# Performance work log

Measured on AMD Instinct MI355X. Metric: run time of the kernel, lower is better.

Reference implementation:

```python
import jax, jax.numpy as jnp
import numpy as np

B, T, D, H = 32, 1024, 128, 4
DH = D // H  # per-head dim = 32
NEG = -(2.0**32) + 1.0  # padding value used by SoftmaxWeightedSum
LN_EPS = 1e-9


def setup_inputs() -> dict:
    key = jax.random.key(0)
    k1, k2, k3, k4 = jax.random.split(key, 4)
    x = jax.random.normal(k1, (B, T, D), dtype=jnp.float32)
    keys_length = jax.random.randint(k2, (B, 1), 1, T + 1, dtype=jnp.int32)
    W = jax.random.normal(k3, (D, 3 * D), dtype=jnp.float32) * 0.05
    W_output = jax.random.normal(k4, (D, D), dtype=jnp.float32) * 0.05
    gamma = jnp.ones((D,), dtype=jnp.float32)
    beta = jnp.zeros((D,), dtype=jnp.float32)
    return {"x": x, "keys_length": keys_length, "W": W,
            "W_output": W_output, "gamma": gamma, "beta": beta}


def reference(x, keys_length, W, W_output, gamma, beta):
    # QKV projection: [B,T,D] @ [D,3D] -> [B,T,3D]
    qkv = jnp.einsum('btd,de->bte', x, W)
    q, k, v = jnp.split(qkv, 3, axis=-1)

    # tf.split(axis=2)+concat(axis=0) == head-major [H,B,T,DH]
    def to_heads(t):
        return t.reshape(B, T, H, DH).transpose(2, 0, 1, 3)
    q, k, v = to_heads(q), to_heads(k), to_heads(v)

    # DotAttention with scale by sqrt(per-head key dim)
    scores = jnp.einsum('hbqd,hbkd->hbqk', q, k) / jnp.sqrt(jnp.float32(DH))

    # key padding mask from sequence lengths: [B,T] bool
    key_mask = jnp.arange(T)[None, :] < keys_length  # keys_length is [B,1]
    # causal (future_binding) lower-triangular mask: [T,T]
    causal = jnp.tril(jnp.ones((T, T), dtype=bool))
    mask = causal[None, None, :, :] & key_mask[None, :, None, :]  # [1,B,T,T] -> broadcast over H
    scores = jnp.where(mask, scores, NEG)

    attn = jax.nn.softmax(scores, axis=-1)  # [H,B,T,T]
    out = jnp.einsum('hbqk,hbkd->hbqd', attn, v)  # [H,B,T,DH]

    # concat heads back to channel dim: [B,T,D]
    out = out.transpose(1, 2, 0, 3).reshape(B, T, D)
    out = jnp.einsum('btd,de->bte', out, W_output)

    # residual + layernorm (dropout is identity at inference)
    out = out + x
    mean = jnp.mean(out, axis=-1, keepdims=True)
    var = jnp.var(out, axis=-1, keepdims=True)
    out = (out - mean) * jax.lax.rsqrt(var + LN_EPS) * gamma + beta
    return out
```

## Files before the change

kernel.cpp:

```cpp
#include <hip/hip_runtime.h>
#include <hip/hip_bf16.h>

#define B_ 32
#define T_ 1024
#define D_ 128
#define H_ 4
#define DH_ 32

typedef unsigned short ushort_t;
typedef unsigned int uint_t;
typedef unsigned short ushort4_t __attribute__((ext_vector_type(4)));
typedef unsigned short ushort8_t __attribute__((ext_vector_type(8)));
typedef short short8_t __attribute__((ext_vector_type(8)));
typedef float float4_t __attribute__((ext_vector_type(4)));

__device__ __forceinline__ ushort_t f2bf_bits(float f) {
    __hip_bfloat16 h = __float2bfloat16(f);
    return *reinterpret_cast<ushort_t*>(&h);
}
__device__ __forceinline__ uint_t pk_bf16(float hi, float lo) {
    return __builtin_amdgcn_perm(__float_as_uint(hi), __float_as_uint(lo),
                                 0x07060302u);
}
#if __has_builtin(__builtin_amdgcn_exp2f)
__device__ __forceinline__ float fast_exp2(float x) { return __builtin_amdgcn_exp2f(x); }
#else
__device__ __forceinline__ float fast_exp2(float x) { return exp2f(x); }
#endif

__global__ __launch_bounds__(256) void transpose_weights(
    const float* __restrict__ W, const float* __restrict__ Wo,
    ushort_t* __restrict__ Wt, ushort_t* __restrict__ Wot)
{
    const int id = blockIdx.x * 256 + threadIdx.x;
    if (id < 128 * 384) {
        const int n = id >> 7, k = id & 127;
        Wt[id] = f2bf_bits(W[(size_t)k * 384 + n]);
    } else {
        const int id2 = id - 128 * 384;
        const int n = id2 >> 7, k = id2 & 127;
        Wot[id2] = f2bf_bits(Wo[(size_t)k * 128 + n]);
    }
}

__global__ __launch_bounds__(256) void qkv_mfma(
    const float* __restrict__ x, const ushort_t* __restrict__ Wt,
    __hip_bfloat16* __restrict__ qws, __hip_bfloat16* __restrict__ kws,
    __hip_bfloat16* __restrict__ vtws)
{
    __shared__ ushort_t qkA[2][16 * 200];
    __shared__ ushort_t qkB[2][16 * 72];

    const int tid = threadIdx.x;
    const int lane = tid & 63;
    const int i15 = lane & 15, quad = lane >> 4;
    const int wid = tid >> 6;
    const int wpart = wid & 1;
    const int pairIdx = wid >> 1;
    const int gw = blockIdx.x * 4 + wid;
    const int row0 = (gw >> 1) * 32;

    short8_t af[2][4];
    #pragma unroll
    for (int rg = 0; rg < 2; ++rg) {
        #pragma unroll
        for (int kc = 0; kc < 4; ++kc) {
            const float4 x0 = *(const float4*)(x + (size_t)(row0 + rg * 16 + i15) * 128 + kc * 32 + quad * 8);
            const float4 x1 = *(const float4*)(x + (size_t)(row0 + rg * 16 + i15) * 128 + kc * 32 + quad * 8 + 4);
            short8_t a;
            a[0] = (short)f2bf_bits(x0.x); a[1] = (short)f2bf_bits(x0.y);
            a[2] = (short)f2bf_bits(x0.z); a[3] = (short)f2bf_bits(x0.w);
            a[4] = (short)f2bf_bits(x1.x); a[5] = (short)f2bf_bits(x1.y);
            a[6] = (short)f2bf_bits(x1.z); a[7] = (short)f2bf_bits(x1.w);
            af[rg][kc] = a;
        }
    }

    float4_t acc[2][12];
    #pragma unroll
    for (int rg = 0; rg < 2; ++rg)
        #pragma unroll
        for (int nt = 0; nt < 12; ++nt) acc[rg][nt] = (float4_t){0.f, 0.f, 0.f, 0.f};

    #pragma unroll
    for (int nt = 0; nt < 12; ++nt) {
        const int n = wpart * 192 + nt * 16 + i15;
        const ushort_t* wb = Wt + (size_t)n * 128 + quad * 8;
        #pragma unroll
        for (int kc = 0; kc < 4; ++kc) {
            const short8_t bf = *(const short8_t*)(wb + kc * 32);
            acc[0][nt] = __builtin_amdgcn_mfma_f32_16x16x32_bf16(af[0][kc], bf, acc[0][nt], 0, 0, 0);
            acc[1][nt] = __builtin_amdgcn_mfma_f32_16x16x32_bf16(af[1][kc], bf, acc[1][nt], 0, 0, 0);
        }
    }

    const float scale = 0.17677669529663687f * 1.4426950408889634f;
    const int t = lane >> 2, c4 = lane & 3;

    #pragma unroll
    for (int rg = 0; rg < 2; ++rg) {
        const int r0 = row0 + rg * 16;
        const int b = r0 >> 10, t0 = r0 & 1023;
        if (wpart == 0) {
            ushort_t* Ls = qkA[pairIdx];
            #pragma unroll
            for (int nt = 0; nt < 12; ++nt) {
                const int col = nt * 16 + i15;
                const float sc = (nt < 8) ? scale : 1.f;
                #pragma unroll
                for (int r = 0; r < 4; ++r)
                    Ls[(quad * 4 + r) * 200 + col] = f2bf_bits(acc[rg][nt][r] * sc);
            }
            #pragma unroll
            for (int it = 0; it < 6; ++it) {
                const int col8 = it * 4 + c4;
                const ushort8_t v8 = *(const ushort8_t*)(Ls + t * 200 + col8 * 8);
                __hip_bfloat16* base = (it < 4) ? qws : kws;
                const int h = (it < 4) ? it : (it - 4);
                *(ushort8_t*)((ushort_t*)base +
                    ((size_t)(b * H_ + h) * T_ + t0 + t) * DH_ + c4 * 8) = v8;
            }
        } else {
            ushort_t* Ls = qkB[pairIdx];
            #pragma unroll
            for (int nt = 0; nt < 12; ++nt) {
                if (nt < 4) {
                    const int col = nt * 16 + i15;
                    #pragma unroll
                    for (int r = 0; r < 4; ++r)
                        Ls[(quad * 4 + r) * 72 + col] = f2bf_bits(acc[rg][nt][r]);
                } else {
                    const int ch = nt * 16 + i15 - 64;
                    const int h = ch >> 5, dh = ch & 31;
                    ushort4_t pk;
                    #pragma unroll
                    for (int r = 0; r < 4; ++r) pk[r] = f2bf_bits(acc[rg][nt][r]);
                    *(ushort4_t*)((ushort_t*)vtws +
                        ((size_t)(b * H_ + h) * DH_ + dh) * T_ + t0 + quad * 4) = pk;
                }
            }
            #pragma unroll
            for (int it = 0; it < 2; ++it) {
                const int col8 = it * 4 + c4;
                const ushort8_t v8 = *(const ushort8_t*)(Ls + t * 72 + col8 * 8);
                *(ushort8_t*)((ushort_t*)kws +
                    ((size_t)(b * H_ + 2 + it) * T_ + t0 + t) * DH_ + c4 * 8) = v8;
            }
        }
    }
}

__global__ __launch_bounds__(256) void attn_proj_ln(
    const ushort_t* __restrict__ qws, const ushort_t* __restrict__ kws,
    const ushort_t* __restrict__ vtws, const int* __restrict__ keys_length,
    const ushort_t* __restrict__ Wot, const float* __restrict__ x,
    const float* __restrict__ gamma, const float* __restrict__ beta,
    float* __restrict__ out)
{
    __shared__ ushort_t plds[4][32 * 72];
    __shared__ ushort_t att[32 * 128];

    const int wid = threadIdx.x >> 6;
    const int lane = threadIdx.x & 63;
    const int i15 = lane & 15, quad = lane >> 4;
    const int b = blockIdx.x & 31;
    const int st = 31 - (blockIdx.x >> 5);
    const int qbase = st * 32;
    const int h = wid;
    const int bh = b * 4 + h;
    const int len = keys_length[b];

    const ushort_t* Qb = qws + (size_t)bh * T_ * DH_;
    const ushort_t* Kb = kws + (size_t)bh * T_ * DH_;
    const ushort_t* Vtb = vtws + (size_t)bh * DH_ * T_;

    const short8_t qfA = *(const short8_t*)(Qb + (size_t)(qbase + i15) * DH_ + quad * 8);
    const short8_t qfB = *(const short8_t*)(Qb + (size_t)(qbase + 16 + i15) * DH_ + quad * 8);

    const int kend    = min(qbase + 32, len);
    const int nch     = (kend + 63) >> 6;
    const int limAmax = min(qbase + 16, len);
    const int nfullA  = min(qbase + 1, len) >> 6;
    const int nfullB  = min(qbase + 17, len) >> 6;
    const int limA    = min(qbase + i15 + 1, len);
    const int limB    = min(qbase + 16 + i15 + 1, len);

    ushort_t* pl = plds[h];

    float4_t oA0 = {0,0,0,0}, oA1 = {0,0,0,0}, oB0 = {0,0,0,0}, oB1 = {0,0,0,0};
    float laccA = 0.f, laccB = 0.f;
    const float4_t zero = {0,0,0,0};

    for (int c = 0; c < nch; ++c) {
        const int k0 = c * 64;
        const bool doA = (k0 < limAmax);

        short8_t kf[4], vf[4];
        #pragma unroll
        for (int g = 0; g < 4; ++g)
            kf[g] = *(const short8_t*)(Kb + (size_t)(k0 + g * 16 + i15) * DH_ + quad * 8);
        vf[0] = *(const short8_t*)(Vtb + (size_t)i15 * T_ + k0 + quad * 8);
        vf[1] = *(const short8_t*)(Vtb + (size_t)i15 * T_ + k0 + 32 + quad * 8);
        vf[2] = *(const short8_t*)(Vtb + (size_t)(16 + i15) * T_ + k0 + quad * 8);
        vf[3] = *(const short8_t*)(Vtb + (size_t)(16 + i15) * T_ + k0 + 32 + quad * 8);

        float4_t sB[4], sA[4];
        #pragma unroll
        for (int g = 0; g < 4; ++g)
            sB[g] = __builtin_amdgcn_mfma_f32_16x16x32_bf16(kf[g], qfB, zero, 0, 0, 0);
        if (doA) {
            #pragma unroll
            for (int g = 0; g < 4; ++g)
                sA[g] = __builtin_amdgcn_mfma_f32_16x16x32_bf16(kf[g], qfA, zero, 0, 0, 0);
        }

        {
            const bool fullB = (c < nfullB);
            ushort_t* prow = pl + (16 + i15) * 72 + quad * 4;
            #pragma unroll
            for (int g = 0; g < 4; ++g) {
                float p0 = fast_exp2(sB[g][0]), p1 = fast_exp2(sB[g][1]);
                float p2 = fast_exp2(sB[g][2]), p3 = fast_exp2(sB[g][3]);
                if (!fullB) {
                    const int d = limB - (k0 + g * 16 + quad * 4);
                    p0 = (d > 0) ? p0 : 0.f; p1 = (d > 1) ? p1 : 0.f;
                    p2 = (d > 2) ? p2 : 0.f; p3 = (d > 3) ? p3 : 0.f;
                }
                laccB += (p0 + p1) + (p2 + p3);
                uint2 w; w.x = pk_bf16(p1, p0); w.y = pk_bf16(p3, p2);
                *(uint2*)(prow + g * 16) = w;
            }
        }
        if (doA) {
            const bool fullA = (c < nfullA);
            ushort_t* prow = pl + i15 * 72 + quad * 4;
            #pragma unroll
            for (int g = 0; g < 4; ++g) {
                float p0 = fast_exp2(sA[g][0]), p1 = fast_exp2(sA[g][1]);
                float p2 = fast_exp2(sA[g][2]), p3 = fast_exp2(sA[g][3]);
                if (!fullA) {
                    const int d = limA - (k0 + g * 16 + quad * 4);
                    p0 = (d > 0) ? p0 : 0.f; p1 = (d > 1) ? p1 : 0.f;
                    p2 = (d > 2) ? p2 : 0.f; p3 = (d > 3) ? p3 : 0.f;
                }
                laccA += (p0 + p1) + (p2 + p3);
                uint2 w; w.x = pk_bf16(p1, p0); w.y = pk_bf16(p3, p2);
                *(uint2*)(prow + g * 16) = w;
            }
        }

        {
            const short8_t pfB0 = *(const short8_t*)(pl + (16 + i15) * 72 + quad * 8);
            const short8_t pfB1 = *(const short8_t*)(pl + (16 + i15) * 72 + 32 + quad * 8);
            oB0 = __builtin_amdgcn_mfma_f32_16x16x32_bf16(pfB0, vf[0], oB0, 0, 0, 0);
            oB0 = __builtin_amdgcn_mfma_f32_16x16x32_bf16(pfB1, vf[1], oB0, 0, 0, 0);
            oB1 = __builtin_amdgcn_mfma_f32_16x16x32_bf16(pfB0, vf[2], oB1, 0, 0, 0);
            oB1 = __builtin_amdgcn_mfma_f32_16x16x32_bf16(pfB1, vf[3], oB1, 0, 0, 0);
        }
        if (doA) {
            const short8_t pfA0 = *(const short8_t*)(pl + i15 * 72 + quad * 8);
            const short8_t pfA1 = *(const short8_t*)(pl + i15 * 72 + 32 + quad * 8);
            oA0 = __builtin_amdgcn_mfma_f32_16x16x32_bf16(pfA0, vf[0], oA0, 0, 0, 0);
            oA0 = __builtin_amdgcn_mfma_f32_16x16x32_bf16(pfA1, vf[1], oA0, 0, 0, 0);
            oA1 = __builtin_amdgcn_mfma_f32_16x16x32_bf16(pfA0, vf[2], oA1, 0, 0, 0);
            oA1 = __builtin_amdgcn_mfma_f32_16x16x32_bf16(pfA1, vf[3], oA1, 0, 0, 0);
        }
    }

    laccA += __shfl_xor(laccA, 16, 64); laccA += __shfl_xor(laccA, 32, 64);
    laccB += __shfl_xor(laccB, 16, 64); laccB += __shfl_xor(laccB, 32, 64);

    #pragma unroll
    for (int r = 0; r < 4; ++r) {
        const int q = quad * 4 + r;
        const float invA = 1.f / __shfl(laccA, q, 64);
        const float invB = 1.f / __shfl(laccB, q, 64);
        const int colL = h * 32 + i15, colH = h * 32 + 16 + i15;
        char* ab = (char*)att;
        *(ushort_t*)(ab + ((q * 256 + colL * 2) ^ ((q & 7) << 4)))        = f2bf_bits(oA0[r] * invA);
        *(ushort_t*)(ab + ((q * 256 + colH * 2) ^ ((q & 7) << 4)))        = f2bf_bits(oA1[r] * invA);
        *(ushort_t*)(ab + (((16 + q) * 256 + colL * 2) ^ ((q & 7) << 4))) = f2bf_bits(oB0[r] * invB);
        *(ushort_t*)(ab + (((16 + q) * 256 + colH * 2) ^ ((q & 7) << 4))) = f2bf_bits(oB1[r] * invB);
    }
    __syncthreads();

    if (wid < 2) {
        const int lr = wid * 16 + i15;
        short8_t af[4];
        #pragma unroll
        for (int kc = 0; kc < 4; ++kc)
            af[kc] = *(const short8_t*)((const char*)att +
                ((lr * 256 + kc * 64 + quad * 16) ^ ((lr & 7) << 4)));

        float4_t acc[8];
        #pragma unroll
        for (int nt = 0; nt < 8; ++nt) acc[nt] = (float4_t){0.f, 0.f, 0.f, 0.f};

        #pragma unroll
        for (int nt = 0; nt < 8; ++nt) {
            const ushort_t* wb = Wot + (size_t)(nt * 16 + i15) * 128 + quad * 8;
            #pragma unroll
            for (int kc = 0; kc < 4; ++kc) {
                const short8_t bf = *(const short8_t*)(wb + kc * 32);
                acc[nt] = __builtin_amdgcn_mfma_f32_16x16x32_bf16(af[kc], bf, acc[nt], 0, 0, 0);
            }
        }

        float g[8], be[8];
        #pragma unroll
        for (int nt = 0; nt < 8; ++nt) {
            g[nt] = gamma[nt * 16 + i15];
            be[nt] = beta[nt * 16 + i15];
        }

        const int m0 = b * T_ + qbase + wid * 16;
        #pragma unroll
        for (int r = 0; r < 4; ++r) {
            const int m = m0 + quad * 4 + r;
            float y[8];
            float s1 = 0.f, s2 = 0.f;
            #pragma unroll
            for (int nt = 0; nt < 8; ++nt) {
                y[nt] = acc[nt][r] + x[(size_t)m * 128 + nt * 16 + i15];
                s1 += y[nt];
                s2 += y[nt] * y[nt];
            }
            #pragma unroll
            for (int off = 1; off < 16; off <<= 1) {
                s1 += __shfl_xor(s1, off, 64);
                s2 += __shfl_xor(s2, off, 64);
            }
            const float mean = s1 * (1.f / 128.f);
            const float var = s2 * (1.f / 128.f) - mean * mean;
            const float rstd = rsqrtf(var + 1e-9f);
            #pragma unroll
            for (int nt = 0; nt < 8; ++nt)
                out[(size_t)m * 128 + nt * 16 + i15] = (y[nt] - mean) * rstd * g[nt] + be[nt];
        }
    }
}

extern "C" void kernel_launch(void* const* d_in, const int* in_sizes, int n_in,
                              void* d_out, int out_size, void* d_ws, size_t ws_size,
                              hipStream_t stream) {
    const float* x      = (const float*)d_in[0];
    const int* keys_len = (const int*)d_in[1];
    const float* W      = (const float*)d_in[2];
    const float* Wo     = (const float*)d_in[3];
    const float* gamma  = (const float*)d_in[4];
    const float* beta   = (const float*)d_in[5];
    float* out          = (float*)d_out;

    const size_t seg = (size_t)B_ * H_ * T_ * DH_;
    __hip_bfloat16* qws  = (__hip_bfloat16*)d_ws;
    __hip_bfloat16* kws  = qws + seg;
    __hip_bfloat16* vtws = qws + 2 * seg;
    ushort_t* Wt  = (ushort_t*)(qws + 3 * seg);
    ushort_t* Wot = Wt + 128 * 384;

    transpose_weights<<<256, 256, 0, stream>>>(W, Wo, Wt, Wot);
    qkv_mfma<<<B_ * T_ / 64, 256, 0, stream>>>(x, Wt, qws, kws, vtws);
    attn_proj_ln<<<B_ * (T_ / 32), 256, 0, stream>>>(
        (const ushort_t*)qws, (const ushort_t*)kws, (const ushort_t*)vtws,
        keys_len, Wot, x, gamma, beta, out);
}
```

Before: 133.4 us.

## Split attention key chunks across two waves per head with register prefetch

New measurement: 143.2 us. 7.4% more time.

```diff
diff --git a/kernel.cpp b/kernel.cpp
--- a/kernel.cpp
+++ b/kernel.cpp
@@ -150,23 +150,24 @@
     }
 }
 
-__global__ __launch_bounds__(256) void attn_proj_ln(
+__global__ __launch_bounds__(512) void attn_proj_ln(
     const ushort_t* __restrict__ qws, const ushort_t* __restrict__ kws,
     const ushort_t* __restrict__ vtws, const int* __restrict__ keys_length,
     const ushort_t* __restrict__ Wot, const float* __restrict__ x,
     const float* __restrict__ gamma, const float* __restrict__ beta,
     float* __restrict__ out)
 {
-    __shared__ ushort_t plds[4][32 * 72];
+    __shared__ ushort_t plds[8][32 * 72];
     __shared__ ushort_t att[32 * 128];
 
     const int wid = threadIdx.x >> 6;
     const int lane = threadIdx.x & 63;
     const int i15 = lane & 15, quad = lane >> 4;
+    const int h = wid >> 1;
+    const int p = wid & 1;
     const int b = blockIdx.x & 31;
     const int st = 31 - (blockIdx.x >> 5);
     const int qbase = st * 32;
-    const int h = wid;
     const int bh = b * 4 + h;
     const int len = keys_length[b];
 
@@ -185,17 +186,15 @@
     const int limA    = min(qbase + i15 + 1, len);
     const int limB    = min(qbase + 16 + i15 + 1, len);
 
-    ushort_t* pl = plds[h];
+    ushort_t* pl = plds[wid];
 
     float4_t oA0 = {0,0,0,0}, oA1 = {0,0,0,0}, oB0 = {0,0,0,0}, oB1 = {0,0,0,0};
     float laccA = 0.f, laccB = 0.f;
     const float4_t zero = {0,0,0,0};
 
-    for (int c = 0; c < nch; ++c) {
-        const int k0 = c * 64;
-        const bool doA = (k0 < limAmax);
-
-        short8_t kf[4], vf[4];
+    short8_t kf[4], vf[4];
+    if (p < nch) {
+        const int k0 = p * 64;
         #pragma unroll
         for (int g = 0; g < 4; ++g)
             kf[g] = *(const short8_t*)(Kb + (size_t)(k0 + g * 16 + i15) * DH_ + quad * 8);
@@ -203,6 +202,11 @@
         vf[1] = *(const short8_t*)(Vtb + (size_t)i15 * T_ + k0 + 32 + quad * 8);
         vf[2] = *(const short8_t*)(Vtb + (size_t)(16 + i15) * T_ + k0 + quad * 8);
         vf[3] = *(const short8_t*)(Vtb + (size_t)(16 + i15) * T_ + k0 + 32 + quad * 8);
+    }
+
+    for (int c = p; c < nch; c += 2) {
+        const int k0 = c * 64;
+        const bool doA = (k0 < limAmax);
 
         float4_t sB[4], sA[4];
         #pragma unroll
@@ -212,6 +216,19 @@
             #pragma unroll
             for (int g = 0; g < 4; ++g)
                 sA[g] = __builtin_amdgcn_mfma_f32_16x16x32_bf16(kf[g], qfA, zero, 0, 0, 0);
+        }
+
+        short8_t kf2[4], vf2[4];
+        const int c2 = c + 2;
+        if (c2 < nch) {
+            const int k2 = c2 * 64;
+            #pragma unroll
+            for (int g = 0; g < 4; ++g)
+                kf2[g] = *(const short8_t*)(Kb + (size_t)(k2 + g * 16 + i15) * DH_ + quad * 8);
+            vf2[0] = *(const short8_t*)(Vtb + (size_t)i15 * T_ + k2 + quad * 8);
+            vf2[1] = *(const short8_t*)(Vtb + (size_t)i15 * T_ + k2 + 32 + quad * 8);
+            vf2[2] = *(const short8_t*)(Vtb + (size_t)(16 + i15) * T_ + k2 + quad * 8);
+            vf2[3] = *(const short8_t*)(Vtb + (size_t)(16 + i15) * T_ + k2 + 32 + quad * 8);
         }
 
         {
@@ -265,22 +282,50 @@
             oA1 = __builtin_amdgcn_mfma_f32_16x16x32_bf16(pfA0, vf[2], oA1, 0, 0, 0);
             oA1 = __builtin_amdgcn_mfma_f32_16x16x32_bf16(pfA1, vf[3], oA1, 0, 0, 0);
         }
+
+        if (c2 < nch) {
+            #pragma unroll
+            for (int g = 0; g < 4; ++g) { kf[g] = kf2[g]; vf[g] = vf2[g]; }
+        }
     }
 
     laccA += __shfl_xor(laccA, 16, 64); laccA += __shfl_xor(laccA, 32, 64);
     laccB += __shfl_xor(laccB, 16, 64); laccB += __shfl_xor(laccB, 32, 64);
 
-    #pragma unroll
-    for (int r = 0; r < 4; ++r) {
-        const int q = quad * 4 + r;
-        const float invA = 1.f / __shfl(laccA, q, 64);
-        const float invB = 1.f / __shfl(laccB, q, 64);
-        const int colL = h * 32 + i15, colH = h * 32 + 16 + i15;
+    __syncthreads();
+    float* comb = (float*)(&plds[0][0]);
+    float* cb = comb + h * 1088;
+    if (p == 0) {
+        #pragma unroll
+        for (int r = 0; r < 4; ++r) {
+            const int q = quad * 4 + r;
+            cb[q * 33 + i15] = oA0[r];
+            cb[q * 33 + 16 + i15] = oA1[r];
+            cb[(16 + q) * 33 + i15] = oB0[r];
+            cb[(16 + q) * 33 + 16 + i15] = oB1[r];
+        }
+        if (quad == 0) { cb[1056 + i15] = laccA; cb[1056 + 16 + i15] = laccB; }
+    }
+    __syncthreads();
+    if (p == 1) {
+        const float lAq = laccA + cb[1056 + i15];
+        const float lBq = laccB + cb[1056 + 16 + i15];
         char* ab = (char*)att;
-        *(ushort_t*)(ab + ((q * 256 + colL * 2) ^ ((q & 7) << 4)))        = f2bf_bits(oA0[r] * invA);
-        *(ushort_t*)(ab + ((q * 256 + colH * 2) ^ ((q & 7) << 4)))        = f2bf_bits(oA1[r] * invA);
-        *(ushort_t*)(ab + (((16 + q) * 256 + colL * 2) ^ ((q & 7) << 4))) = f2bf_bits(oB0[r] * invB);
-        *(ushort_t*)(ab + (((16 + q) * 256 + colH * 2) ^ ((q & 7) << 4))) = f2bf_bits(oB1[r] * invB);
+        #pragma unroll
+        for (int r = 0; r < 4; ++r) {
+            const int q = quad * 4 + r;
+            const float invA = 1.f / __shfl(lAq, q, 64);
+            const float invB = 1.f / __shfl(lBq, q, 64);
+            const float a0 = oA0[r] + cb[q * 33 + i15];
+            const float a1 = oA1[r] + cb[q * 33 + 16 + i15];
+            const float b0 = oB0[r] + cb[(16 + q) * 33 + i15];
+            const float b1 = oB1[r] + cb[(16 + q) * 33 + 16 + i15];
+            const int colL = h * 32 + i15, colH = h * 32 + 16 + i15;
+            *(ushort_t*)(ab + ((q * 256 + colL * 2) ^ ((q & 7) << 4)))        = f2bf_bits(a0 * invA);
+            *(ushort_t*)(ab + ((q * 256 + colH * 2) ^ ((q & 7) << 4)))        = f2bf_bits(a1 * invA);
+            *(ushort_t*)(ab + (((16 + q) * 256 + colL * 2) ^ ((q & 7) << 4))) = f2bf_bits(b0 * invB);
+            *(ushort_t*)(ab + (((16 + q) * 256 + colH * 2) ^ ((q & 7) << 4))) = f2bf_bits(b1 * invB);
+        }
     }
     __syncthreads();
 
@@ -360,7 +405,7 @@
 
     transpose_weights<<<256, 256, 0, stream>>>(W, Wo, Wt, Wot);
     qkv_mfma<<<B_ * T_ / 64, 256, 0, stream>>>(x, Wt, qws, kws, vtws);
-    attn_proj_ln<<<B_ * (T_ / 32), 256, 0, stream>>>(
+    attn_proj_ln<<<B_ * (T_ / 32), 512, 0, stream>>>(
         (const ushort_t*)qws, (const ushort_t*)kws, (const ushort_t*)vtws,
         keys_len, Wot, x, gamma, beta, out);
 }
```

## Prefetch K/V and weight tiles, halve QKV rows per wave, add MFMA priority

Applied to the files above, without the earlier changes.

Result: slower. 141.5 us (+6.1%).

```diff
diff --git a/kernel.cpp b/kernel.cpp
--- a/kernel.cpp
+++ b/kernel.cpp
@@ -58,94 +58,96 @@
     const int wpart = wid & 1;
     const int pairIdx = wid >> 1;
     const int gw = blockIdx.x * 4 + wid;
-    const int row0 = (gw >> 1) * 32;
-
-    short8_t af[2][4];
+    const int row0 = (gw >> 1) * 16;
+    const int b = row0 >> 10, t0 = row0 & 1023;
+
+    short8_t af[4];
     #pragma unroll
-    for (int rg = 0; rg < 2; ++rg) {
-        #pragma unroll
-        for (int kc = 0; kc < 4; ++kc) {
-            const float4 x0 = *(const float4*)(x + (size_t)(row0 + rg * 16 + i15) * 128 + kc * 32 + quad * 8);
-            const float4 x1 = *(const float4*)(x + (size_t)(row0 + rg * 16 + i15) * 128 + kc * 32 + quad * 8 + 4);
-            short8_t a;
-            a[0] = (short)f2bf_bits(x0.x); a[1] = (short)f2bf_bits(x0.y);
-            a[2] = (short)f2bf_bits(x0.z); a[3] = (short)f2bf_bits(x0.w);
-            a[4] = (short)f2bf_bits(x1.x); a[5] = (short)f2bf_bits(x1.y);
-            a[6] = (short)f2bf_bits(x1.z); a[7] = (short)f2bf_bits(x1.w);
-            af[rg][kc] = a;
-        }
-    }
-
-    float4_t acc[2][12];
+    for (int kc = 0; kc < 4; ++kc) {
+        const float4 x0 = *(const float4*)(x + (size_t)(row0 + i15) * 128 + kc * 32 + quad * 8);
+        const float4 x1 = *(const float4*)(x + (size_t)(row0 + i15) * 128 + kc * 32 + quad * 8 + 4);
+        short8_t a;
+        a[0] = (short)f2bf_bits(x0.x); a[1] = (short)f2bf_bits(x0.y);
+        a[2] = (short)f2bf_bits(x0.z); a[3] = (short)f2bf_bits(x0.w);
+        a[4] = (short)f2bf_bits(x1.x); a[5] = (short)f2bf_bits(x1.y);
+        a[6] = (short)f2bf_bits(x1.z); a[7] = (short)f2bf_bits(x1.w);
+        af[kc] = a;
+    }
+
+    float4_t acc[12];
     #pragma unroll
-    for (int rg = 0; rg < 2; ++rg)
-        #pragma unroll
-        for (int nt = 0; nt < 12; ++nt) acc[rg][nt] = (float4_t){0.f, 0.f, 0.f, 0.f};
-
+    for (int nt = 0; nt < 12; ++nt) acc[nt] = (float4_t){0.f, 0.f, 0.f, 0.f};
+
+    short8_t bcur[4], bnext[4];
+    {
+        const ushort_t* wb = Wt + (size_t)(wpart * 192 + i15) * 128 + quad * 8;
+        #pragma unroll
+        for (int kc = 0; kc < 4; ++kc) bcur[kc] = *(const short8_t*)(wb + kc * 32);
+    }
     #pragma unroll
     for (int nt = 0; nt < 12; ++nt) {
-        const int n = wpart * 192 + nt * 16 + i15;
-        const ushort_t* wb = Wt + (size_t)n * 128 + quad * 8;
-        #pragma unroll
-        for (int kc = 0; kc < 4; ++kc) {
-            const short8_t bf = *(const short8_t*)(wb + kc * 32);
-            acc[0][nt] = __builtin_amdgcn_mfma_f32_16x16x32_bf16(af[0][kc], bf, acc[0][nt], 0, 0, 0);
-            acc[1][nt] = __builtin_amdgcn_mfma_f32_16x16x32_bf16(af[1][kc], bf, acc[1][nt], 0, 0, 0);
+        if (nt < 11) {
+            const ushort_t* wbn = Wt + (size_t)(wpart * 192 + (nt + 1) * 16 + i15) * 128 + quad * 8;
+            #pragma unroll
+            for (int kc = 0; kc < 4; ++kc) bnext[kc] = *(const short8_t*)(wbn + kc * 32);
+        }
+        #pragma unroll
+        for (int kc = 0; kc < 4; ++kc)
+            acc[nt] = __builtin_amdgcn_mfma_f32_16x16x32_bf16(af[kc], bcur[kc], acc[nt], 0, 0, 0);
+        if (nt < 11) {
+            #pragma unroll
+            for (int kc = 0; kc < 4; ++kc) bcur[kc] = bnext[kc];
         }
     }
 
     const float scale = 0.17677669529663687f * 1.4426950408889634f;
-    const int t = lane >> 2, c4 = lane & 3;
-
-    #pragma unroll
-    for (int rg = 0; rg < 2; ++rg) {
-        const int r0 = row0 + rg * 16;
-        const int b = r0 >> 10, t0 = r0 & 1023;
-        if (wpart == 0) {
-            ushort_t* Ls = qkA[pairIdx];
-            #pragma unroll
-            for (int nt = 0; nt < 12; ++nt) {
+
+    if (wpart == 0) {
+        ushort_t* Ls = qkA[pairIdx];
+        #pragma unroll
+        for (int nt = 0; nt < 12; ++nt) {
+            const int col = nt * 16 + i15;
+            const float sc = (nt < 8) ? scale : 1.f;
+            #pragma unroll
+            for (int r = 0; r < 4; ++r)
+                Ls[(quad * 4 + r) * 200 + col] = f2bf_bits(acc[nt][r] * sc);
+        }
+        const int t = lane >> 2, c4 = lane & 3;
+        #pragma unroll
+        for (int it = 0; it < 6; ++it) {
+            const int col8 = it * 4 + c4;
+            const ushort8_t v8 = *(const ushort8_t*)(Ls + t * 200 + col8 * 8);
+            __hip_bfloat16* base = (it < 4) ? qws : kws;
+            const int h = (it < 4) ? it : (it - 4);
+            *(ushort8_t*)((ushort_t*)base +
+                ((size_t)(b * H_ + h) * T_ + t0 + t) * DH_ + c4 * 8) = v8;
+        }
+    } else {
+        ushort_t* Ls = qkB[pairIdx];
+        #pragma unroll
+        for (int nt = 0; nt < 12; ++nt) {
+            if (nt < 4) {
                 const int col = nt * 16 + i15;
-                const float sc = (nt < 8) ? scale : 1.f;
                 #pragma unroll
                 for (int r = 0; r < 4; ++r)
-                    Ls[(quad * 4 + r) * 200 + col] = f2bf_bits(acc[rg][nt][r] * sc);
-            }
-            #pragma unroll
-            for (int it = 0; it < 6; ++it) {
-                const int col8 = it * 4 + c4;
-                const ushort8_t v8 = *(const ushort8_t*)(Ls + t * 200 + col8 * 8);
-                __hip_bfloat16* base = (it < 4) ? qws : kws;
-                const int h = (it < 4) ? it : (it - 4);
-                *(ushort8_t*)((ushort_t*)base +
-                    ((size_t)(b * H_ + h) * T_ + t0 + t) * DH_ + c4 * 8) = v8;
-            }
-        } else {
-            ushort_t* Ls = qkB[pairIdx];
-            #pragma unroll
-            for (int nt = 0; nt < 12; ++nt) {
-                if (nt < 4) {
-                    const int col = nt * 16 + i15;
-                    #pragma unroll
-                    for (int r = 0; r < 4; ++r)
-                        Ls[(quad * 4 + r) * 72 + col] = f2bf_bits(acc[rg][nt][r]);
-                } else {
-                    const int ch = nt * 16 + i15 - 64;
-                    const int h = ch >> 5, dh = ch & 31;
-                    ushort4_t pk;
-                    #pragma unroll
-                    for (int r = 0; r < 4; ++r) pk[r] = f2bf_bits(acc[rg][nt][r]);
-                    *(ushort4_t*)((ushort_t*)vtws +
-                        ((size_t)(b * H_ + h) * DH_ + dh) * T_ + t0 + quad * 4) = pk;
-                }
-            }
-            #pragma unroll
-            for (int it = 0; it < 2; ++it) {
-                const int col8 = it * 4 + c4;
-                const ushort8_t v8 = *(const ushort8_t*)(Ls + t * 72 + col8 * 8);
-                *(ushort8_t*)((ushort_t*)kws +
-                    ((size_t)(b * H_ + 2 + it) * T_ + t0 + t) * DH_ + c4 * 8) = v8;
-            }
+                    Ls[(quad * 4 + r) * 72 + col] = f2bf_bits(acc[nt][r]);
+            } else {
+                const int ch = nt * 16 + i15 - 64;
+                const int h = ch >> 5, dh = ch & 31;
+                ushort4_t pk;
+                #pragma unroll
+                for (int r = 0; r < 4; ++r) pk[r] = f2bf_bits(acc[nt][r]);
+                *(ushort4_t*)((ushort_t*)vtws +
+                    ((size_t)(b * H_ + h) * DH_ + dh) * T_ + t0 + quad * 4) = pk;
+            }
+        }
+        const int t = lane >> 2, c4 = lane & 3;
+        #pragma unroll
+        for (int it = 0; it < 2; ++it) {
+            const int col8 = it * 4 + c4;
+            const ushort8_t v8 = *(const ushort8_t*)(Ls + t * 72 + col8 * 8);
+            *(ushort8_t*)((ushort_t*)kws +
+                ((size_t)(b * H_ + 2 + it) * T_ + t0 + t) * DH_ + c4 * 8) = v8;
         }
     }
 }
@@ -191,20 +193,21 @@
     float laccA = 0.f, laccB = 0.f;
     const float4_t zero = {0,0,0,0};
 
+    short8_t kf[4], vf[4];
+    #pragma unroll
+    for (int g = 0; g < 4; ++g)
+        kf[g] = *(const short8_t*)(Kb + (size_t)(g * 16 + i15) * DH_ + quad * 8);
+    vf[0] = *(const short8_t*)(Vtb + (size_t)i15 * T_ + quad * 8);
+    vf[1] = *(const short8_t*)(Vtb + (size_t)i15 * T_ + 32 + quad * 8);
+    vf[2] = *(const short8_t*)(Vtb + (size_t)(16 + i15) * T_ + quad * 8);
+    vf[3] = *(const short8_t*)(Vtb + (size_t)(16 + i15) * T_ + 32 + quad * 8);
+
     for (int c = 0; c < nch; ++c) {
         const int k0 = c * 64;
         const bool doA = (k0 < limAmax);
 
-        short8_t kf[4], vf[4];
-        #pragma unroll
-        for (int g = 0; g < 4; ++g)
-            kf[g] = *(const short8_t*)(Kb + (size_t)(k0 + g * 16 + i15) * DH_ + quad * 8);
-        vf[0] = *(const short8_t*)(Vtb + (size_t)i15 * T_ + k0 + quad * 8);
-        vf[1] = *(const short8_t*)(Vtb + (size_t)i15 * T_ + k0 + 32 + quad * 8);
-        vf[2] = *(const short8_t*)(Vtb + (size_t)(16 + i15) * T_ + k0 + quad * 8);
-        vf[3] = *(const short8_t*)(Vtb + (size_t)(16 + i15) * T_ + k0 + 32 + quad * 8);
-
         float4_t sB[4], sA[4];
+        __builtin_amdgcn_s_setprio(1);
         #pragma unroll
         for (int g = 0; g < 4; ++g)
             sB[g] = __builtin_amdgcn_mfma_f32_16x16x32_bf16(kf[g], qfB, zero, 0, 0, 0);
@@ -212,6 +215,20 @@
             #pragma unroll
             for (int g = 0; g < 4; ++g)
                 sA[g] = __builtin_amdgcn_mfma_f32_16x16x32_bf16(kf[g], qfA, zero, 0, 0, 0);
+        }
+        __builtin_amdgcn_s_setprio(0);
+
+        short8_t kf2[4], vf2[4];
+        const int c2 = c + 1;
+        if (c2 < nch) {
+            const int k2 = c2 * 64;
+            #pragma unroll
+            for (int g = 0; g < 4; ++g)
+                kf2[g] = *(const short8_t*)(Kb + (size_t)(k2 + g * 16 + i15) * DH_ + quad * 8);
+            vf2[0] = *(const short8_t*)(Vtb + (size_t)i15 * T_ + k2 + quad * 8);
+            vf2[1] = *(const short8_t*)(Vtb + (size_t)i15 * T_ + k2 + 32 + quad * 8);
+            vf2[2] = *(const short8_t*)(Vtb + (size_t)(16 + i15) * T_ + k2 + quad * 8);
+            vf2[3] = *(const short8_t*)(Vtb + (size_t)(16 + i15) * T_ + k2 + 32 + quad * 8);
         }
 
         {
@@ -249,6 +266,7 @@
             }
         }
 
+        __builtin_amdgcn_s_setprio(1);
         {
             const short8_t pfB0 = *(const short8_t*)(pl + (16 + i15) * 72 + quad * 8);
             const short8_t pfB1 = *(const short8_t*)(pl + (16 + i15) * 72 + 32 + quad * 8);
@@ -264,6 +282,12 @@
             oA0 = __builtin_amdgcn_mfma_f32_16x16x32_bf16(pfA1, vf[1], oA0, 0, 0, 0);
             oA1 = __builtin_amdgcn_mfma_f32_16x16x32_bf16(pfA0, vf[2], oA1, 0, 0, 0);
             oA1 = __builtin_amdgcn_mfma_f32_16x16x32_bf16(pfA1, vf[3], oA1, 0, 0, 0);
+        }
+        __builtin_amdgcn_s_setprio(0);
+
+        if (c2 < nch) {
+            #pragma unroll
+            for (int g = 0; g < 4; ++g) { kf[g] = kf2[g]; vf[g] = vf2[g]; }
         }
     }
 
@@ -282,6 +306,16 @@
         *(ushort_t*)(ab + (((16 + q) * 256 + colL * 2) ^ ((q & 7) << 4))) = f2bf_bits(oB0[r] * invB);
         *(ushort_t*)(ab + (((16 + q) * 256 + colH * 2) ^ ((q & 7) << 4))) = f2bf_bits(oB1[r] * invB);
     }
+
+    float xr[4][8];
+    if (wid < 2) {
+        const int m0 = b * T_ + qbase + wid * 16;
+        #pragma unroll
+        for (int r = 0; r < 4; ++r)
+            #pragma unroll
+            for (int nt = 0; nt < 8; ++nt)
+                xr[r][nt] = x[(size_t)(m0 + quad * 4 + r) * 128 + nt * 16 + i15];
+    }
     __syncthreads();
 
     if (wid < 2) {
@@ -321,7 +355,7 @@
             float s1 = 0.f, s2 = 0.f;
             #pragma unroll
             for (int nt = 0; nt < 8; ++nt) {
-                y[nt] = acc[nt][r] + x[(size_t)m * 128 + nt * 16 + i15];
+                y[nt] = acc[nt][r] + xr[r][nt];
                 s1 += y[nt];
                 s2 += y[nt] * y[nt];
             }
@@ -359,7 +393,7 @@
     ushort_t* Wot = Wt + 128 * 384;
 
     transpose_weights<<<256, 256, 0, stream>>>(W, Wo, Wt, Wot);
-    qkv_mfma<<<B_ * T_ / 64, 256, 0, stream>>>(x, Wt, qws, kws, vtws);
+    qkv_mfma<<<B_ * T_ / 32, 256, 0, stream>>>(x, Wt, qws, kws, vtws);
     attn_proj_ln<<<B_ * (T_ / 32), 256, 0, stream>>>(
         (const ushort_t*)qws, (const ushort_t*)kws, (const ushort_t*)vtws,
         keys_len, Wot, x, gamma, beta, out);
```

## Prefetch next K chunk, raise MFMA priority, split output projection across four waves

Applied to the files above, without the earlier changes.

Result: no change. 135.9 us (+1.9%).

```diff
diff --git a/kernel.cpp b/kernel.cpp
--- a/kernel.cpp
+++ b/kernel.cpp
@@ -191,20 +191,23 @@
     float laccA = 0.f, laccB = 0.f;
     const float4_t zero = {0,0,0,0};
 
+    short8_t kf[4];
+    #pragma unroll
+    for (int g = 0; g < 4; ++g)
+        kf[g] = *(const short8_t*)(Kb + (size_t)(g * 16 + i15) * DH_ + quad * 8);
+
     for (int c = 0; c < nch; ++c) {
         const int k0 = c * 64;
         const bool doA = (k0 < limAmax);
 
-        short8_t kf[4], vf[4];
-        #pragma unroll
-        for (int g = 0; g < 4; ++g)
-            kf[g] = *(const short8_t*)(Kb + (size_t)(k0 + g * 16 + i15) * DH_ + quad * 8);
+        short8_t vf[4];
         vf[0] = *(const short8_t*)(Vtb + (size_t)i15 * T_ + k0 + quad * 8);
         vf[1] = *(const short8_t*)(Vtb + (size_t)i15 * T_ + k0 + 32 + quad * 8);
         vf[2] = *(const short8_t*)(Vtb + (size_t)(16 + i15) * T_ + k0 + quad * 8);
         vf[3] = *(const short8_t*)(Vtb + (size_t)(16 + i15) * T_ + k0 + 32 + quad * 8);
 
         float4_t sB[4], sA[4];
+        __builtin_amdgcn_s_setprio(1);
         #pragma unroll
         for (int g = 0; g < 4; ++g)
             sB[g] = __builtin_amdgcn_mfma_f32_16x16x32_bf16(kf[g], qfB, zero, 0, 0, 0);
@@ -212,6 +215,16 @@
             #pragma unroll
             for (int g = 0; g < 4; ++g)
                 sA[g] = __builtin_amdgcn_mfma_f32_16x16x32_bf16(kf[g], qfA, zero, 0, 0, 0);
+        }
+        __builtin_amdgcn_s_setprio(0);
+
+        short8_t kf2[4];
+        const int c2 = c + 1;
+        if (c2 < nch) {
+            const int k2 = c2 * 64;
+            #pragma unroll
+            for (int g = 0; g < 4; ++g)
+                kf2[g] = *(const short8_t*)(Kb + (size_t)(k2 + g * 16 + i15) * DH_ + quad * 8);
         }
 
         {
@@ -249,6 +262,7 @@
             }
         }
 
+        __builtin_amdgcn_s_setprio(1);
         {
             const short8_t pfB0 = *(const short8_t*)(pl + (16 + i15) * 72 + quad * 8);
             const short8_t pfB1 = *(const short8_t*)(pl + (16 + i15) * 72 + 32 + quad * 8);
@@ -264,6 +278,12 @@
             oA0 = __builtin_amdgcn_mfma_f32_16x16x32_bf16(pfA1, vf[1], oA0, 0, 0, 0);
             oA1 = __builtin_amdgcn_mfma_f32_16x16x32_bf16(pfA0, vf[2], oA1, 0, 0, 0);
             oA1 = __builtin_amdgcn_mfma_f32_16x16x32_bf16(pfA1, vf[3], oA1, 0, 0, 0);
+        }
+        __builtin_amdgcn_s_setprio(0);
+
+        if (c2 < nch) {
+            #pragma unroll
+            for (int g = 0; g < 4; ++g) kf[g] = kf2[g];
         }
     }
 
@@ -284,21 +304,22 @@
     }
     __syncthreads();
 
-    if (wid < 2) {
-        const int lr = wid * 16 + i15;
+    {
+        const int ch = wid >> 1, rh = wid & 1;
+        const int lr = rh * 16 + i15;
         short8_t af[4];
         #pragma unroll
         for (int kc = 0; kc < 4; ++kc)
             af[kc] = *(const short8_t*)((const char*)att +
                 ((lr * 256 + kc * 64 + quad * 16) ^ ((lr & 7) << 4)));
 
-        float4_t acc[8];
-        #pragma unroll
-        for (int nt = 0; nt < 8; ++nt) acc[nt] = (float4_t){0.f, 0.f, 0.f, 0.f};
-
-        #pragma unroll
-        for (int nt = 0; nt < 8; ++nt) {
-            const ushort_t* wb = Wot + (size_t)(nt * 16 + i15) * 128 + quad * 8;
+        float4_t acc[4];
+        #pragma unroll
+        for (int nt = 0; nt < 4; ++nt) acc[nt] = (float4_t){0.f, 0.f, 0.f, 0.f};
+
+        #pragma unroll
+        for (int nt = 0; nt < 4; ++nt) {
+            const ushort_t* wb = Wot + (size_t)((ch * 4 + nt) * 16 + i15) * 128 + quad * 8;
             #pragma unroll
             for (int kc = 0; kc < 4; ++kc) {
                 const short8_t bf = *(const short8_t*)(wb + kc * 32);
@@ -306,36 +327,48 @@
             }
         }
 
-        float g[8], be[8];
-        #pragma unroll
-        for (int nt = 0; nt < 8; ++nt) {
-            g[nt] = gamma[nt * 16 + i15];
-            be[nt] = beta[nt * 16 + i15];
-        }
-
-        const int m0 = b * T_ + qbase + wid * 16;
+        float g[4], be[4];
+        #pragma unroll
+        for (int nt = 0; nt < 4; ++nt) {
+            g[nt] = gamma[ch * 64 + nt * 16 + i15];
+            be[nt] = beta[ch * 64 + nt * 16 + i15];
+        }
+
+        float y[4][4], s1r[4], s2r[4];
+        const int m0 = b * T_ + qbase + rh * 16;
+        float2* pbuf = (float2*)(&plds[0][0]);
         #pragma unroll
         for (int r = 0; r < 4; ++r) {
             const int m = m0 + quad * 4 + r;
-            float y[8];
             float s1 = 0.f, s2 = 0.f;
             #pragma unroll
-            for (int nt = 0; nt < 8; ++nt) {
-                y[nt] = acc[nt][r] + x[(size_t)m * 128 + nt * 16 + i15];
-                s1 += y[nt];
-                s2 += y[nt] * y[nt];
+            for (int nt = 0; nt < 4; ++nt) {
+                y[r][nt] = acc[nt][r] + x[(size_t)m * 128 + ch * 64 + nt * 16 + i15];
+                s1 += y[r][nt];
+                s2 += y[r][nt] * y[r][nt];
             }
             #pragma unroll
             for (int off = 1; off < 16; off <<= 1) {
                 s1 += __shfl_xor(s1, off, 64);
                 s2 += __shfl_xor(s2, off, 64);
             }
+            s1r[r] = s1; s2r[r] = s2;
+            if (i15 == 0)
+                pbuf[ch * 32 + rh * 16 + quad * 4 + r] = (float2){s1, s2};
+        }
+        __syncthreads();
+        #pragma unroll
+        for (int r = 0; r < 4; ++r) {
+            const int m = m0 + quad * 4 + r;
+            const float2 o = pbuf[(1 - ch) * 32 + rh * 16 + quad * 4 + r];
+            const float s1 = s1r[r] + o.x, s2 = s2r[r] + o.y;
             const float mean = s1 * (1.f / 128.f);
             const float var = s2 * (1.f / 128.f) - mean * mean;
             const float rstd = rsqrtf(var + 1e-9f);
             #pragma unroll
-            for (int nt = 0; nt < 8; ++nt)
-                out[(size_t)m * 128 + nt * 16 + i15] = (y[nt] - mean) * rstd * g[nt] + be[nt];
+            for (int nt = 0; nt < 4; ++nt)
+                out[(size_t)m * 128 + ch * 64 + nt * 16 + i15] =
+                    (y[r][nt] - mean) * rstd * g[nt] + be[nt];
         }
     }
 }
```
